# Kernel tuning notes

Hardware: AMD Instinct MI355X
Metric: run time of the kernel (lower is better)

Reference implementation:

```python
import jax, jax.numpy as jnp
import numpy as np

NUM_HEADS = 4
HEAD_DIM = 64


def _leaky(v):
    return jnp.where(v > 0, v, 0.01 * v)


def setup_inputs() -> dict:
    key = jax.random.key(0)
    ks = jax.random.split(key, 13)
    N, C, D, H, W = 8, 2, 2048, 16, 16
    return {
        "x": jax.random.normal(ks[0], (N, C, D, H, W), jnp.float32),
        "conv1_w": jax.random.normal(ks[1], (64, C), jnp.float32) * 0.3,
        "bn_gamma": jax.random.uniform(ks[2], (64,), jnp.float32, 0.5, 1.5),
        "bn_beta": jax.random.normal(ks[3], (64,), jnp.float32) * 0.1,
        "bn_mean": jax.random.normal(ks[4], (64,), jnp.float32) * 0.1,
        "bn_var": jax.random.uniform(ks[5], (64,), jnp.float32, 0.5, 1.5),
        "conv2_w": jax.random.normal(ks[6], (64, 64), jnp.float32) * 0.125,
        "ln_w": jax.random.uniform(ks[7], (64, D), jnp.float32, 0.5, 1.5),
        "ln_b": jax.random.normal(ks[8], (64, D), jnp.float32) * 0.1,
        "w_q": jax.random.normal(ks[9], (NUM_HEADS * HEAD_DIM, 64), jnp.float32) * 0.125,
        "w_k": jax.random.normal(ks[10], (NUM_HEADS * HEAD_DIM, 64), jnp.float32) * 0.125,
        "w_v": jax.random.normal(ks[11], (NUM_HEADS * HEAD_DIM, 64), jnp.float32) * 0.125,
        "w_out": jax.random.normal(ks[12], (1, NUM_HEADS * HEAD_DIM), jnp.float32) * 0.0625,
    }


def reference(x, conv1_w, bn_gamma, bn_beta, bn_mean, bn_var, conv2_w,
              ln_w, ln_b, w_q, w_k, w_v, w_out):
    N, C, D, H, W = x.shape
    nh, dh = NUM_HEADS, HEAD_DIM

    # gap: AdaptiveAvgPool3d([D,1,1]) with input depth == windows_size == D
    t = x.mean(axis=(3, 4))                             # [N, C, D]
    # merge_channel: 1x1 Conv3d (C->64), BN (eval), LeakyReLU, 1x1 Conv3d (64->64), LayerNorm
    t = jnp.einsum('ncd,oc->nod', t, conv1_w)           # [N, 64, D]
    inv = bn_gamma / jnp.sqrt(bn_var + 1e-5)
    t = _leaky(t * inv[None, :, None] + (bn_beta - bn_mean * inv)[None, :, None])
    t = jnp.einsum('ncd,oc->nod', t, conv2_w)           # [N, 64, D]
    mu = t.mean(axis=(1, 2), keepdims=True)
    var = ((t - mu) ** 2).mean(axis=(1, 2), keepdims=True)
    t = (t - mu) / jnp.sqrt(var + 1e-6) * ln_w[None] + ln_b[None]
    t = t.transpose(0, 2, 1)                            # [N, D, 64]

    # Q/K/V projections and head split (chunk along dim 2, cat along dim 0)
    Q = t @ w_q.T                                       # [N, D, nh*dh]
    K = t @ w_k.T
    V = t @ w_v.T
    Qh = Q.reshape(N, D, nh, dh).transpose(2, 0, 1, 3)  # [nh, N, D, dh]
    Kh = K.reshape(N, D, nh, dh).transpose(2, 0, 1, 3)
    Vh = V.reshape(N, D, nh, dh).transpose(2, 0, 1, 3)

    # scaled dot-product attention (note: scaled by d_k, not sqrt(d_k), as in source)
    scores = jnp.einsum('hnqd,hnkd->hnqk', Qh, Kh) / dh # [nh, N, D, D]
    mask = jnp.tril(jnp.ones((D, D), bool))
    scores = jnp.where(mask[None, None], scores, -jnp.inf)
    att = jax.nn.softmax(scores, axis=-1)               # [nh, N, D, D]
    out = jnp.einsum('hnqk,hnkd->hnqd', att, Vh)        # [nh, N, D, dh]

    att_values = out.transpose(1, 2, 0, 3).reshape(N, D, nh * dh)  # [N, D, 256]
    att_merge = att_values @ w_out.T                    # [N, D, 1]

    inputs_ = x.transpose(0, 2, 1, 3, 4).reshape(N, D, C * H * W)  # [N, D, C*H*W]
    y = (inputs_ * att_merge).reshape(N, D, C, H, W).transpose(0, 2, 1, 3, 4)
    att_softmax = att.reshape(nh * N, D, D)
    return (y, att_softmax, att_values, att_merge)
```

## Files before the change

### kernel.cpp

```cpp
#include <hip/hip_runtime.h>

typedef __attribute__((ext_vector_type(8))) short short8;
typedef __attribute__((ext_vector_type(4))) float f32x4;

#define MFMA16(a, b, c) __builtin_amdgcn_mfma_f32_16x16x32_bf16((a), (b), (c), 0, 0, 0)

static __device__ __forceinline__ unsigned short f2bf(float x) {
    unsigned int u = __builtin_bit_cast(unsigned int, x);
    unsigned int r = (u + 0x7FFFu + ((u >> 16) & 1u)) >> 16;
    return (unsigned short)r;
}
static __device__ __forceinline__ float bf2f(unsigned short h) {
    unsigned int u = ((unsigned int)h) << 16;
    return __builtin_bit_cast(float, u);
}

__global__ void k_init(float* stats) {
    if (threadIdx.x < 16) stats[threadIdx.x] = 0.0f;
}

__global__ void k_gap(const float* __restrict__ x, float* __restrict__ t0) {
    int wv = threadIdx.x >> 6, l = threadIdx.x & 63;
    int row = blockIdx.x * 4 + wv;
    float4 v = *(const float4*)(x + (size_t)row * 256 + l * 4);
    float s = v.x + v.y + v.z + v.w;
    #pragma unroll
    for (int m = 1; m < 64; m <<= 1) s += __shfl_xor(s, m, 64);
    if (l == 0) t0[row] = s * (1.0f / 256.0f);
}

__global__ void k_merge(const float* __restrict__ t0, const float* __restrict__ w1,
                        const float* __restrict__ gamma, const float* __restrict__ beta,
                        const float* __restrict__ mean, const float* __restrict__ var,
                        const float* __restrict__ w2, float* __restrict__ t2,
                        float* __restrict__ stats) {
    __shared__ float w2s[64][65];
    int tid = threadIdx.x, wv = tid >> 6, o = tid & 63;
    int n = blockIdx.y, d0 = blockIdx.x * 32;
    for (int i = tid; i < 4096; i += 256) w2s[i >> 6][i & 63] = w2[i];
    float w10 = w1[o * 2], w11 = w1[o * 2 + 1];
    float inv = gamma[o] * rsqrtf(var[o] + 1e-5f);
    float b2 = beta[o] - mean[o] * inv;
    __syncthreads();
    float ssum = 0.0f, ssq = 0.0f;
    for (int i = 0; i < 8; ++i) {
        int d = d0 + wv * 8 + i;
        float a = t0[(n * 2 + 0) * 2048 + d];
        float b = t0[(n * 2 + 1) * 2048 + d];
        float h = (w10 * a + w11 * b) * inv + b2;
        h = h > 0.0f ? h : 0.01f * h;
        float acc = 0.0f;
        for (int c = 0; c < 64; ++c) acc += w2s[o][c] * __shfl(h, c, 64);
        t2[((size_t)n * 2048 + d) * 64 + o] = acc;
        ssum += acc; ssq += acc * acc;
    }
    #pragma unroll
    for (int m = 1; m < 64; m <<= 1) {
        ssum += __shfl_xor(ssum, m, 64);
        ssq  += __shfl_xor(ssq, m, 64);
    }
    if (o == 0) { atomicAdd(&stats[n * 2], ssum); atomicAdd(&stats[n * 2 + 1], ssq); }
}

__global__ __launch_bounds__(256) void k_qkv(
        const float* __restrict__ t2, const float* __restrict__ stats,
        const float* __restrict__ lnw, const float* __restrict__ lnb,
        const float* __restrict__ wq, const float* __restrict__ wk, const float* __restrict__ wvp,
        unsigned short* __restrict__ Qhi, unsigned short* __restrict__ Qlo,
        unsigned short* __restrict__ Khi, unsigned short* __restrict__ Klo,
        unsigned short* __restrict__ Vthi, unsigned short* __restrict__ Vtlo) {
    __shared__ float tl[16][64];
    __shared__ __align__(16) unsigned short vth[256][16];
    __shared__ __align__(16) unsigned short vtl[256][16];
    int tid = threadIdx.x;
    int n = blockIdx.y, d0 = blockIdx.x * 16;
    float mu = stats[n * 2] * (1.0f / 131072.0f);
    float ex2 = stats[n * 2 + 1] * (1.0f / 131072.0f);
    float rstd = rsqrtf(ex2 - mu * mu + 1e-6f);
    {
        int dd = tid >> 4, c0 = (tid & 15) * 4;
        float4 v = *(const float4*)(t2 + ((size_t)n * 2048 + d0 + dd) * 64 + c0);
        float vv[4] = {v.x, v.y, v.z, v.w};
        #pragma unroll
        for (int j = 0; j < 4; ++j) {
            int c = c0 + j;
            tl[dd][c] = (vv[j] - mu) * rstd * lnw[c * 2048 + d0 + dd] + lnb[c * 2048 + d0 + dd];
        }
    }
    __syncthreads();
    int o = tid;
    float aq[16], ak[16], av[16];
    #pragma unroll
    for (int d = 0; d < 16; ++d) { aq[d] = 0; ak[d] = 0; av[d] = 0; }
    for (int c = 0; c < 64; ++c) {
        float wqc = wq[o * 64 + c], wkc = wk[o * 64 + c], wvc = wvp[o * 64 + c];
        #pragma unroll
        for (int d = 0; d < 16; ++d) {
            float t = tl[d][c];
            aq[d] += wqc * t; ak[d] += wkc * t; av[d] += wvc * t;
        }
    }
    int h = o >> 6, dd2 = o & 63;
    size_t hn = (size_t)h * 8 + n;
    #pragma unroll
    for (int d = 0; d < 16; ++d) {
        size_t base = (hn * 2048 + d0 + d) * 64 + dd2;
        unsigned short qh = f2bf(aq[d]); Qhi[base] = qh; Qlo[base] = f2bf(aq[d] - bf2f(qh));
        unsigned short kh = f2bf(ak[d]); Khi[base] = kh; Klo[base] = f2bf(ak[d] - bf2f(kh));
        unsigned short vh = f2bf(av[d]); vth[o][d] = vh; vtl[o][d] = f2bf(av[d] - bf2f(vh));
    }
    __syncthreads();
    {
        size_t vrow = (hn * 64 + dd2) * 2048 + d0;
        uint4 a0 = *(uint4*)&vth[o][0];
        uint4 a1 = *(uint4*)&vth[o][8];
        *(uint4*)(Vthi + vrow) = a0;
        *(uint4*)(Vthi + vrow + 8) = a1;
        uint4 b0 = *(uint4*)&vtl[o][0];
        uint4 b1 = *(uint4*)&vtl[o][8];
        *(uint4*)(Vtlo + vrow) = b0;
        *(uint4*)(Vtlo + vrow + 8) = b1;
    }
}

__global__ __launch_bounds__(256) void k_attn(
        const unsigned short* __restrict__ Qhi, const unsigned short* __restrict__ Qlo,
        const unsigned short* __restrict__ Khi, const unsigned short* __restrict__ Klo,
        const unsigned short* __restrict__ Vthi, const unsigned short* __restrict__ Vtlo,
        float* __restrict__ att, float* __restrict__ attv) {
    __shared__ __align__(16) unsigned char smem[49152];
    int tid = threadIdx.x;
    int wv = tid >> 6, l = tid & 63;
    int lo4 = l & 15, hi4 = l >> 4;
    int hn = blockIdx.x;
    int qt = 31 - blockIdx.y;
    int q0 = qt * 64, qw = q0 + wv * 16;
    size_t qkbase = (size_t)hn * 2048 * 64;

    short8 qfh[2], qfl[2];
    {
        int qrow = qw + lo4;
        #pragma unroll
        for (int ks = 0; ks < 2; ++ks) {
            size_t a = qkbase + (size_t)qrow * 64 + ks * 32 + hi4 * 8;
            qfh[ks] = *(const short8*)(Qhi + a);
            qfl[ks] = *(const short8*)(Qlo + a);
        }
    }

    float lsum[4] = {0, 0, 0, 0};
    for (int kt = 0; kt <= qt; ++kt) {
        __syncthreads();
        #pragma unroll
        for (int rep = 0; rep < 2; ++rep) {
            int task = rep * 256 + tid;
            int kk = task >> 3, c = task & 7;
            int sw = kk * 128 + ((c * 16) ^ ((kk & 7) << 4));
            size_t g = qkbase + (size_t)(kt * 64 + kk) * 64 + c * 8;
            *(short8*)(smem + sw) = *(const short8*)(Khi + g);
            *(short8*)(smem + 8192 + sw) = *(const short8*)(Klo + g);
        }
        __syncthreads();
        #pragma unroll
        for (int n16 = 0; n16 < 4; ++n16) {
            f32x4 acc = {0.f, 0.f, 0.f, 0.f};
            int kk = n16 * 16 + lo4;
            #pragma unroll
            for (int ks = 0; ks < 2; ++ks) {
                int sw = kk * 128 + ((ks * 64 + hi4 * 16) ^ ((kk & 7) << 4));
                short8 kfh = *(const short8*)(smem + sw);
                short8 kfl = *(const short8*)(smem + 8192 + sw);
                acc = MFMA16(qfh[ks], kfh, acc);
                acc = MFMA16(qfh[ks], kfl, acc);
                acc = MFMA16(qfl[ks], kfh, acc);
            }
            int col = kt * 64 + n16 * 16 + lo4;
            #pragma unroll
            for (int r = 0; r < 4; ++r) {
                int row = qw + hi4 * 4 + r;
                if (col <= row) lsum[r] += __expf(acc[r] * 0.015625f);
            }
        }
    }
    float linv[4];
    #pragma unroll
    for (int r = 0; r < 4; ++r) {
        float s = lsum[r];
        s += __shfl_xor(s, 1, 64); s += __shfl_xor(s, 2, 64);
        s += __shfl_xor(s, 4, 64); s += __shfl_xor(s, 8, 64);
        linv[r] = 1.0f / s;
    }

    f32x4 onn[4];
    #pragma unroll
    for (int i = 0; i < 4; ++i) onn[i] = (f32x4){0.f, 0.f, 0.f, 0.f};
    unsigned char* pbh = smem + 32768 + wv * 4096;
    unsigned char* pbl = pbh + 2048;

    for (int kt = 0; kt <= qt; ++kt) {
        __syncthreads();
        #pragma unroll
        for (int rep = 0; rep < 2; ++rep) {
            int task = rep * 256 + tid;
            int kk = task >> 3, c = task & 7;
            int sw = kk * 128 + ((c * 16) ^ ((kk & 7) << 4));
            size_t g = qkbase + (size_t)(kt * 64 + kk) * 64 + c * 8;
            *(short8*)(smem + sw) = *(const short8*)(Khi + g);
            *(short8*)(smem + 8192 + sw) = *(const short8*)(Klo + g);
            size_t gv = ((size_t)hn * 64 + kk) * 2048 + kt * 64 + c * 8;
            *(short8*)(smem + 16384 + sw) = *(const short8*)(Vthi + gv);
            *(short8*)(smem + 24576 + sw) = *(const short8*)(Vtlo + gv);
        }
        __syncthreads();
        #pragma unroll
        for (int n16 = 0; n16 < 4; ++n16) {
            f32x4 acc = {0.f, 0.f, 0.f, 0.f};
            int kk = n16 * 16 + lo4;
            #pragma unroll
            for (int ks = 0; ks < 2; ++ks) {
                int sw = kk * 128 + ((ks * 64 + hi4 * 16) ^ ((kk & 7) << 4));
                short8 kfh = *(const short8*)(smem + sw);
                short8 kfl = *(const short8*)(smem + 8192 + sw);
                acc = MFMA16(qfh[ks], kfh, acc);
                acc = MFMA16(qfh[ks], kfl, acc);
                acc = MFMA16(qfl[ks], kfh, acc);
            }
            #pragma unroll
            for (int r = 0; r < 4; ++r) {
                int row = qw + hi4 * 4 + r;
                int col = kt * 64 + n16 * 16 + lo4;
                float p = 0.0f;
                if (col <= row) p = __expf(acc[r] * 0.015625f) * linv[r];
                att[((size_t)(hn * 2048 + row)) * 2048 + col] = p;
                unsigned short ph = f2bf(p);
                unsigned short pl = f2bf(p - bf2f(ph));
                int prow = hi4 * 4 + r;
                int pby = prow * 128 + (((n16 * 16 + lo4) * 2) ^ ((prow & 7) << 4));
                *(unsigned short*)(pbh + pby) = ph;
                *(unsigned short*)(pbl + pby) = pl;
            }
        }
        short8 pfh[2], pfl[2];
        #pragma unroll
        for (int ks = 0; ks < 2; ++ks) {
            int pby = lo4 * 128 + ((ks * 64 + hi4 * 16) ^ ((lo4 & 7) << 4));
            pfh[ks] = *(const short8*)(pbh + pby);
            pfl[ks] = *(const short8*)(pbl + pby);
        }
        #pragma unroll
        for (int dd16 = 0; dd16 < 4; ++dd16) {
            #pragma unroll
            for (int ks = 0; ks < 2; ++ks) {
                int vrow = dd16 * 16 + lo4;
                int vby = vrow * 128 + ((ks * 64 + hi4 * 16) ^ ((vrow & 7) << 4));
                short8 vfh = *(const short8*)(smem + 16384 + vby);
                short8 vfl = *(const short8*)(smem + 24576 + vby);
                onn[dd16] = MFMA16(vfh, pfh[ks], onn[dd16]);
                onn[dd16] = MFMA16(vfh, pfl[ks], onn[dd16]);
                onn[dd16] = MFMA16(vfl, pfh[ks], onn[dd16]);
            }
        }
    }

    {
        int n_ = hn & 7, h_ = hn >> 3;
        int q = qw + lo4;
        #pragma unroll
        for (int dd16 = 0; dd16 < 4; ++dd16) {
            size_t a = ((size_t)n_ * 2048 + q) * 256 + h_ * 64 + dd16 * 16 + hi4 * 4;
            *(f32x4*)(attv + a) = onn[dd16];
        }
    }

    float4 z4 = make_float4(0.f, 0.f, 0.f, 0.f);
    for (int r = 0; r < 64; ++r) {
        size_t rowbase = ((size_t)(hn * 2048 + q0 + r)) * 2048;
        for (int c = q0 + 64 + tid * 4; c < 2048; c += 1024) {
            *(float4*)(att + rowbase + c) = z4;
        }
    }
}

__global__ void k_avmerge(const float* __restrict__ attv, const float* __restrict__ wout,
                          float* __restrict__ amerge) {
    int wv = threadIdx.x >> 6, l = threadIdx.x & 63;
    int row = blockIdx.x * 4 + wv;
    float4 a = *(const float4*)(attv + (size_t)row * 256 + l * 4);
    float4 w = *(const float4*)(wout + l * 4);
    float s = a.x * w.x + a.y * w.y + a.z * w.z + a.w * w.w;
    #pragma unroll
    for (int m = 1; m < 64; m <<= 1) s += __shfl_xor(s, m, 64);
    if (l == 0) amerge[row] = s;
}

__global__ void k_y(const float* __restrict__ x, const float* __restrict__ amerge,
                    float* __restrict__ y) {
    size_t i = (size_t)blockIdx.x * 256 + threadIdx.x;
    for (size_t idx = i; idx < 2097152; idx += 524288) {
        size_t row = idx >> 6;
        int n = (int)(row >> 12);
        int d = (int)(row & 2047);
        float am = amerge[n * 2048 + d];
        float4 v = *(const float4*)(x + idx * 4);
        v.x *= am; v.y *= am; v.z *= am; v.w *= am;
        *(float4*)(y + idx * 4) = v;
    }
}

extern "C" void kernel_launch(void* const* d_in, const int* in_sizes, int n_in,
                              void* d_out, int out_size, void* d_ws, size_t ws_size,
                              hipStream_t stream) {
    const float* x        = (const float*)d_in[0];
    const float* conv1_w  = (const float*)d_in[1];
    const float* bn_gamma = (const float*)d_in[2];
    const float* bn_beta  = (const float*)d_in[3];
    const float* bn_mean  = (const float*)d_in[4];
    const float* bn_var   = (const float*)d_in[5];
    const float* conv2_w  = (const float*)d_in[6];
    const float* ln_w     = (const float*)d_in[7];
    const float* ln_b     = (const float*)d_in[8];
    const float* w_q      = (const float*)d_in[9];
    const float* w_k      = (const float*)d_in[10];
    const float* w_v      = (const float*)d_in[11];
    const float* w_out    = (const float*)d_in[12];

    float* ws = (float*)d_ws;
    float* stats = ws;
    float* t0 = ws + 16;
    float* t2 = ws + 16 + 32768;
    unsigned short* ub = (unsigned short*)(ws + 1081360);
    const size_t B = 4194304;
    unsigned short* Qhi = ub;
    unsigned short* Qlo = ub + B;
    unsigned short* Khi = ub + 2 * B;
    unsigned short* Klo = ub + 3 * B;
    unsigned short* Vthi = ub + 4 * B;
    unsigned short* Vtlo = ub + 5 * B;

    float* out = (float*)d_out;
    float* y = out;
    float* att = out + 8388608;
    float* attv = out + 142606336;
    float* amerge = out + 146800640;

    hipLaunchKernelGGL(k_init, dim3(1), dim3(64), 0, stream, stats);
    hipLaunchKernelGGL(k_gap, dim3(8192), dim3(256), 0, stream, x, t0);
    hipLaunchKernelGGL(k_merge, dim3(64, 8), dim3(256), 0, stream,
                       t0, conv1_w, bn_gamma, bn_beta, bn_mean, bn_var, conv2_w, t2, stats);
    hipLaunchKernelGGL(k_qkv, dim3(128, 8), dim3(256), 0, stream,
                       t2, stats, ln_w, ln_b, w_q, w_k, w_v,
                       Qhi, Qlo, Khi, Klo, Vthi, Vtlo);
    hipLaunchKernelGGL(k_attn, dim3(32, 32), dim3(256), 0, stream,
                       Qhi, Qlo, Khi, Klo, Vthi, Vtlo, att, attv);
    hipLaunchKernelGGL(k_avmerge, dim3(4096), dim3(256), 0, stream, attv, w_out, amerge);
    hipLaunchKernelGGL(k_y, dim3(2048), dim3(256), 0, stream, x, amerge, y);
}
```

Measured before the change: 987.2 us.

## Prefetch K/V tiles into registers, transpose QKV weights, use nontemporal stores

The attention kernel now loads the next K/V tile into registers while the current tile is being computed, so global load latency overlaps the MFMA work, and it sets a launch-bounds occupancy hint of 3. The QKV weights are transposed once by a new small kernel so the projection kernel reads coalesced weight columns. The large att and y outputs are written with nontemporal stores to reduce cache pollution. Holding the prefetched tiles in registers raises register pressure, and the occupancy hint could force spills.

```diff
diff --git a/kernel.cpp b/kernel.cpp
--- a/kernel.cpp
+++ b/kernel.cpp
@@ -27,6 +27,20 @@
     #pragma unroll
     for (int m = 1; m < 64; m <<= 1) s += __shfl_xor(s, m, 64);
     if (l == 0) t0[row] = s * (1.0f / 256.0f);
+}
+
+__global__ void k_wt(const float* __restrict__ wq, const float* __restrict__ wk,
+                     const float* __restrict__ wv, float* __restrict__ wqT,
+                     float* __restrict__ wkT, float* __restrict__ wvT) {
+    const float* s; float* d;
+    if (blockIdx.x == 0)      { s = wq; d = wqT; }
+    else if (blockIdx.x == 1) { s = wk; d = wkT; }
+    else                      { s = wv; d = wvT; }
+    for (int i = threadIdx.x; i < 2048; i += 256) {
+        int idx = blockIdx.y * 2048 + i;
+        int o = idx >> 6, c = idx & 63;
+        d[c * 256 + o] = s[idx];
+    }
 }
 
 __global__ void k_merge(const float* __restrict__ t0, const float* __restrict__ w1,
@@ -65,7 +79,7 @@
 __global__ __launch_bounds__(256) void k_qkv(
         const float* __restrict__ t2, const float* __restrict__ stats,
         const float* __restrict__ lnw, const float* __restrict__ lnb,
-        const float* __restrict__ wq, const float* __restrict__ wk, const float* __restrict__ wvp,
+        const float* __restrict__ wqT, const float* __restrict__ wkT, const float* __restrict__ wvT,
         unsigned short* __restrict__ Qhi, unsigned short* __restrict__ Qlo,
         unsigned short* __restrict__ Khi, unsigned short* __restrict__ Klo,
         unsigned short* __restrict__ Vthi, unsigned short* __restrict__ Vtlo) {
@@ -93,7 +107,7 @@
     #pragma unroll
     for (int d = 0; d < 16; ++d) { aq[d] = 0; ak[d] = 0; av[d] = 0; }
     for (int c = 0; c < 64; ++c) {
-        float wqc = wq[o * 64 + c], wkc = wk[o * 64 + c], wvc = wvp[o * 64 + c];
+        float wqc = wqT[c * 256 + o], wkc = wkT[c * 256 + o], wvc = wvT[c * 256 + o];
         #pragma unroll
         for (int d = 0; d < 16; ++d) {
             float t = tl[d][c];
@@ -123,7 +137,7 @@
     }
 }
 
-__global__ __launch_bounds__(256) void k_attn(
+__global__ __launch_bounds__(256, 3) void k_attn(
         const unsigned short* __restrict__ Qhi, const unsigned short* __restrict__ Qlo,
         const unsigned short* __restrict__ Khi, const unsigned short* __restrict__ Klo,
         const unsigned short* __restrict__ Vthi, const unsigned short* __restrict__ Vtlo,
@@ -137,6 +151,14 @@
     int q0 = qt * 64, qw = q0 + wv * 16;
     size_t qkbase = (size_t)hn * 2048 * 64;
 
+    const int kk0 = tid >> 3, c0s = tid & 7;
+    const int sw0 = kk0 * 128 + ((c0s * 16) ^ ((kk0 & 7) << 4));
+    const int sw1 = sw0 + 4096;
+    const size_t gK0 = qkbase + (size_t)kk0 * 64 + c0s * 8;
+    const size_t gK1 = gK0 + 32 * 64;
+    const size_t gV0 = (size_t)hn * 64 * 2048 + (size_t)kk0 * 2048 + c0s * 8;
+    const size_t gV1 = gV0 + 32 * 2048;
+
     short8 qfh[2], qfl[2];
     {
         int qrow = qw + lo4;
@@ -148,17 +170,22 @@
         }
     }
 
+    short8 skh0, skh1, skl0, skl1;
+    short8 svh0, svh1, svl0, svl1;
+
     float lsum[4] = {0, 0, 0, 0};
+    {
+        skh0 = *(const short8*)(Khi + gK0); skh1 = *(const short8*)(Khi + gK1);
+        skl0 = *(const short8*)(Klo + gK0); skl1 = *(const short8*)(Klo + gK1);
+    }
     for (int kt = 0; kt <= qt; ++kt) {
         __syncthreads();
-        #pragma unroll
-        for (int rep = 0; rep < 2; ++rep) {
-            int task = rep * 256 + tid;
-            int kk = task >> 3, c = task & 7;
-            int sw = kk * 128 + ((c * 16) ^ ((kk & 7) << 4));
-            size_t g = qkbase + (size_t)(kt * 64 + kk) * 64 + c * 8;
-            *(short8*)(smem + sw) = *(const short8*)(Khi + g);
-            *(short8*)(smem + 8192 + sw) = *(const short8*)(Klo + g);
+        *(short8*)(smem + sw0) = skh0;        *(short8*)(smem + sw1) = skh1;
+        *(short8*)(smem + 8192 + sw0) = skl0; *(short8*)(smem + 8192 + sw1) = skl1;
+        if (kt < qt) {
+            size_t o = (size_t)(kt + 1) * 4096;
+            skh0 = *(const short8*)(Khi + gK0 + o); skh1 = *(const short8*)(Khi + gK1 + o);
+            skl0 = *(const short8*)(Klo + gK0 + o); skl1 = *(const short8*)(Klo + gK1 + o);
         }
         __syncthreads();
         #pragma unroll
@@ -182,6 +209,13 @@
             }
         }
     }
+
+    {
+        skh0 = *(const short8*)(Khi + gK0); skh1 = *(const short8*)(Khi + gK1);
+        skl0 = *(const short8*)(Klo + gK0); skl1 = *(const short8*)(Klo + gK1);
+        svh0 = *(const short8*)(Vthi + gV0); svh1 = *(const short8*)(Vthi + gV1);
+        svl0 = *(const short8*)(Vtlo + gV0); svl1 = *(const short8*)(Vtlo + gV1);
+    }
     float linv[4];
     #pragma unroll
     for (int r = 0; r < 4; ++r) {
@@ -199,17 +233,17 @@
 
     for (int kt = 0; kt <= qt; ++kt) {
         __syncthreads();
-        #pragma unroll
-        for (int rep = 0; rep < 2; ++rep) {
-            int task = rep * 256 + tid;
-            int kk = task >> 3, c = task & 7;
-            int sw = kk * 128 + ((c * 16) ^ ((kk & 7) << 4));
-            size_t g = qkbase + (size_t)(kt * 64 + kk) * 64 + c * 8;
-            *(short8*)(smem + sw) = *(const short8*)(Khi + g);
-            *(short8*)(smem + 8192 + sw) = *(const short8*)(Klo + g);
-            size_t gv = ((size_t)hn * 64 + kk) * 2048 + kt * 64 + c * 8;
-            *(short8*)(smem + 16384 + sw) = *(const short8*)(Vthi + gv);
-            *(short8*)(smem + 24576 + sw) = *(const short8*)(Vtlo + gv);
+        *(short8*)(smem + sw0) = skh0;         *(short8*)(smem + sw1) = skh1;
+        *(short8*)(smem + 8192 + sw0) = skl0;  *(short8*)(smem + 8192 + sw1) = skl1;
+        *(short8*)(smem + 16384 + sw0) = svh0; *(short8*)(smem + 16384 + sw1) = svh1;
+        *(short8*)(smem + 24576 + sw0) = svl0; *(short8*)(smem + 24576 + sw1) = svl1;
+        if (kt < qt) {
+            size_t o = (size_t)(kt + 1) * 4096;
+            size_t ov = (size_t)(kt + 1) * 64;
+            skh0 = *(const short8*)(Khi + gK0 + o); skh1 = *(const short8*)(Khi + gK1 + o);
+            skl0 = *(const short8*)(Klo + gK0 + o); skl1 = *(const short8*)(Klo + gK1 + o);
+            svh0 = *(const short8*)(Vthi + gV0 + ov); svh1 = *(const short8*)(Vthi + gV1 + ov);
+            svl0 = *(const short8*)(Vtlo + gV0 + ov); svl1 = *(const short8*)(Vtlo + gV1 + ov);
         }
         __syncthreads();
         #pragma unroll
@@ -231,7 +265,7 @@
                 int col = kt * 64 + n16 * 16 + lo4;
                 float p = 0.0f;
                 if (col <= row) p = __expf(acc[r] * 0.015625f) * linv[r];
-                att[((size_t)(hn * 2048 + row)) * 2048 + col] = p;
+                __builtin_nontemporal_store(p, att + ((size_t)(hn * 2048 + row)) * 2048 + col);
                 unsigned short ph = f2bf(p);
                 unsigned short pl = f2bf(p - bf2f(ph));
                 int prow = hi4 * 4 + r;
@@ -272,11 +306,11 @@
         }
     }
 
-    float4 z4 = make_float4(0.f, 0.f, 0.f, 0.f);
+    f32x4 z4 = {0.f, 0.f, 0.f, 0.f};
     for (int r = 0; r < 64; ++r) {
         size_t rowbase = ((size_t)(hn * 2048 + q0 + r)) * 2048;
         for (int c = q0 + 64 + tid * 4; c < 2048; c += 1024) {
-            *(float4*)(att + rowbase + c) = z4;
+            __builtin_nontemporal_store(z4, (f32x4*)(att + rowbase + c));
         }
     }
 }
@@ -301,9 +335,9 @@
         int n = (int)(row >> 12);
         int d = (int)(row & 2047);
         float am = amerge[n * 2048 + d];
-        float4 v = *(const float4*)(x + idx * 4);
-        v.x *= am; v.y *= am; v.z *= am; v.w *= am;
-        *(float4*)(y + idx * 4) = v;
+        f32x4 v = *(const f32x4*)(x + idx * 4);
+        v *= am;
+        __builtin_nontemporal_store(v, (f32x4*)(y + idx * 4));
     }
 }
 
@@ -328,7 +362,10 @@
     float* stats = ws;
     float* t0 = ws + 16;
     float* t2 = ws + 16 + 32768;
-    unsigned short* ub = (unsigned short*)(ws + 1081360);
+    float* wqT = ws + 1081360;
+    float* wkT = wqT + 16384;
+    float* wvT = wkT + 16384;
+    unsigned short* ub = (unsigned short*)(wvT + 16384);
     const size_t B = 4194304;
     unsigned short* Qhi = ub;
     unsigned short* Qlo = ub + B;
@@ -344,11 +381,13 @@
     float* amerge = out + 146800640;
 
     hipLaunchKernelGGL(k_init, dim3(1), dim3(64), 0, stream, stats);
+    hipLaunchKernelGGL(k_wt, dim3(3, 8), dim3(256), 0, stream,
+                       w_q, w_k, w_v, wqT, wkT, wvT);
     hipLaunchKernelGGL(k_gap, dim3(8192), dim3(256), 0, stream, x, t0);
     hipLaunchKernelGGL(k_merge, dim3(64, 8), dim3(256), 0, stream,
                        t0, conv1_w, bn_gamma, bn_beta, bn_mean, bn_var, conv2_w, t2, stats);
     hipLaunchKernelGGL(k_qkv, dim3(128, 8), dim3(256), 0, stream,
-                       t2, stats, ln_w, ln_b, w_q, w_k, w_v,
+                       t2, stats, ln_w, ln_b, wqT, wkT, wvT,
                        Qhi, Qlo, Khi, Klo, Vthi, Vtlo);
     hipLaunchKernelGGL(k_attn, dim3(32, 32), dim3(256), 0, stream,
                        Qhi, Qlo, Khi, Klo, Vthi, Vtlo, att, attv);
```

Result: faster. 848.0 us (-14.1%).
